# Optimization experiments

Hardware: AMD Instinct MI355X
Metric: run time of the kernel (lower is better)

Reference implementation:

```python
import jax, jax.numpy as jnp
import numpy as np

ALPHA = 0.2  # LeakyReLU negative slope
B, L, FIN, FOUT = 128, 512, 128, 128

def setup_inputs() -> dict:
    key = jax.random.key(0)
    k1, k2, k3, k4, k5 = jax.random.split(key, 5)
    h = jax.random.normal(k1, (B, L, FIN), jnp.float32)
    W = jax.random.normal(k2, (FIN, FOUT), jnp.float32) * (1.0 / np.sqrt(FIN))
    a = jax.random.normal(k3, (2 * FOUT,), jnp.float32) * (1.0 / np.sqrt(2 * FOUT))
    edge_bias = jax.random.normal(k4, (B, L, L), jnp.float32) * 0.1
    adj_mask = jax.random.uniform(k5, (L, L)) > 0.3
    adj_mask = adj_mask | jnp.eye(L, dtype=bool)  # self-loops avoid fully-masked rows
    return {"h": h, "W": W, "a": a, "edge_bias": edge_bias, "adj_mask": adj_mask}

def reference(h, W, a, edge_bias, adj_mask):
    # Wh: [B, L, Fout]
    Wh = jnp.einsum('blf,fo->blo', h, W)
    Fout = W.shape[1]
    # a([Wh_i, Wh_j]) == Wh_i @ a[:Fout] + Wh_j @ a[Fout:]  (avoids O(B*L*L*2F) concat)
    ei = Wh @ a[:Fout]   # [B, L]  (target i contribution)
    ej = Wh @ a[Fout:]   # [B, L]  (source j contribution)
    e = jax.nn.leaky_relu(ei[:, :, None] + ej[:, None, :], ALPHA) + edge_bias  # [B, L, L]
    e = jnp.where(adj_mask[None, :, :], e, -jnp.inf)
    att = jax.nn.softmax(e, axis=-1)  # dropout=0.0 -> identity
    h_prime = jnp.einsum('bij,bjo->bio', att, Wh)  # [B, L, Fout]
    return jax.nn.elu(h_prime)  # concat=True branch
```

## Files before the change

### kernel.cpp

```cpp
#include <hip/hip_runtime.h>
#include <string.h>

#define ALPHA 0.2f

typedef short short8 __attribute__((ext_vector_type(8)));
typedef float floatx4 __attribute__((ext_vector_type(4)));
typedef unsigned short ushort8 __attribute__((ext_vector_type(8)));

__device__ inline unsigned short f2bf(float f) {
    unsigned int v; __builtin_memcpy(&v, &f, 4);
    v = v + 0x7FFFu + ((v >> 16) & 1u);
    return (unsigned short)(v >> 16);
}
__device__ inline float bf2f(unsigned short u) {
    unsigned int v = ((unsigned int)u) << 16;
    float f; __builtin_memcpy(&f, &v, 4); return f;
}

__global__ __launch_bounds__(256) void wh_kernel(const float* __restrict__ h,
                                                 const float* __restrict__ W,
                                                 const float* __restrict__ a,
                                                 unsigned short* __restrict__ wht,
                                                 float* __restrict__ ei,
                                                 float* __restrict__ ej)
{
    __shared__ __align__(16) unsigned short w_t[128][136];
    __shared__ __align__(16) unsigned short out_s[128][136];
    const int tid  = threadIdx.x;
    const int lane = tid & 63;
    const int wv   = tid >> 6;
    const int quad = lane >> 4;
    const int l16  = lane & 15;
    const int r0   = blockIdx.x * 128;
    const int b    = r0 >> 9;
    const int jb   = r0 & 511;

    for (int k = 0; k < 64; ++k) {
        int idx = k * 256 + tid;
        w_t[idx & 127][idx >> 7] = f2bf(W[idx]);
    }
    float a1v[8], a2v[8];
    for (int n = 0; n < 8; ++n) {
        a1v[n] = a[n * 16 + l16];
        a2v[n] = a[128 + n * 16 + l16];
    }
    __syncthreads();

    floatx4 acc[2][8];
    for (int m = 0; m < 2; ++m)
        for (int n = 0; n < 8; ++n) acc[m][n] = (floatx4)0.f;

    for (int kk = 0; kk < 4; ++kk) {
        short8 afr[2];
        for (int m = 0; m < 2; ++m) {
            int r = r0 + wv * 32 + m * 16 + l16;
            const float* src = h + r * 128 + kk * 32 + quad * 8;
            short8 t;
            for (int e = 0; e < 8; ++e) t[e] = (short)f2bf(src[e]);
            afr[m] = t;
        }
        for (int n = 0; n < 8; ++n) {
            short8 bfr = *(const short8*)(&w_t[n * 16 + l16][kk * 32 + quad * 8]);
            for (int m = 0; m < 2; ++m)
                acc[m][n] = __builtin_amdgcn_mfma_f32_16x16x32_bf16(afr[m], bfr, acc[m][n], 0, 0, 0);
        }
    }

    for (int m = 0; m < 2; ++m)
        for (int r = 0; r < 4; ++r) {
            float si = 0.f, sj = 0.f;
            for (int n = 0; n < 8; ++n) {
                float v = acc[m][n][r];
                si += v * a1v[n];
                sj += v * a2v[n];
            }
            for (int off = 8; off; off >>= 1) {
                si += __shfl_xor(si, off);
                sj += __shfl_xor(sj, off);
            }
            if (l16 == 0) {
                int il = wv * 32 + m * 16 + quad * 4 + r;
                ei[b * 512 + jb + il] = si;
                ej[b * 512 + jb + il] = sj;
            }
        }

    for (int m = 0; m < 2; ++m)
        for (int n = 0; n < 8; ++n)
            for (int r = 0; r < 4; ++r)
                out_s[wv * 32 + m * 16 + quad * 4 + r][n * 16 + l16] = f2bf(acc[m][n][r]);
    __syncthreads();

    for (int it = 0; it < 8; ++it) {
        int vid = it * 256 + tid;
        int o   = vid >> 4;
        int jv  = (vid & 15) * 8;
        ushort8 tmp;
        for (int e = 0; e < 8; ++e) tmp[e] = out_s[jv + e][o];
        *(ushort8*)(wht + b * 65536 + o * 512 + jb + jv) = tmp;
    }
}

__global__ __launch_bounds__(256) void attn_kernel(const unsigned short* __restrict__ wht,
                                                   const float* __restrict__ ei,
                                                   const float* __restrict__ ej,
                                                   const float* __restrict__ bias,
                                                   const int* __restrict__ adj,
                                                   float* __restrict__ out)
{
    __shared__ __align__(16) unsigned short p_s[32][520];
    __shared__ __align__(16) unsigned short wh_s[128][136];
    __shared__ float ej_s[512];
    __shared__ float ei_s[32];
    __shared__ float s_row[32];

    const int tid  = threadIdx.x;
    const int lane = tid & 63;
    const int wv   = tid >> 6;
    const int quad = lane >> 4;
    const int l16  = lane & 15;
    const int b    = blockIdx.x >> 4;
    const int i0   = (blockIdx.x & 15) * 32;

    ej_s[tid]       = ej[b * 512 + tid];
    ej_s[256 + tid] = ej[b * 512 + 256 + tid];
    if (tid < 32) ei_s[tid] = ei[b * 512 + i0 + tid];
    __syncthreads();

    for (int rr = 0; rr < 8; ++rr) {
        int il = wv * 8 + rr;
        int ig = i0 + il;
        float eiv = ei_s[il];
        const float* brow = bias + (size_t)(((b << 9) + ig)) * 512;
        const int* arow = adj + (ig << 9);
        float e8[8];
        float mx = -1e30f;
        for (int q = 0; q < 8; ++q) {
            int j = q * 64 + lane;
            float x = eiv + ej_s[j];
            x = x > 0.f ? x : ALPHA * x;
            x += brow[j];
            if (arow[j] == 0) x = -1e30f;
            e8[q] = x;
            mx = fmaxf(mx, x);
        }
        for (int off = 32; off; off >>= 1) mx = fmaxf(mx, __shfl_xor(mx, off));
        float sm = 0.f;
        for (int q = 0; q < 8; ++q) {
            float p = __expf(e8[q] - mx);
            p_s[il][q * 64 + lane] = f2bf(p);
            sm += p;
        }
        for (int off = 32; off; off >>= 1) sm += __shfl_xor(sm, off);
        if (lane == 0) s_row[il] = sm;
    }
    __syncthreads();

    floatx4 acc[2][2];
    for (int m = 0; m < 2; ++m)
        for (int n = 0; n < 2; ++n) acc[m][n] = (floatx4)0.f;

    for (int kc = 0; kc < 4; ++kc) {
        __syncthreads();
        for (int it = 0; it < 8; ++it) {
            int vid = it * 256 + tid;
            int o   = vid >> 4;
            int jv  = (vid & 15) * 8;
            *(ushort8*)&wh_s[o][jv] =
                *(const ushort8*)(wht + b * 65536 + o * 512 + kc * 128 + jv);
        }
        __syncthreads();
        for (int ks = 0; ks < 4; ++ks) {
            int ko = ks * 32 + quad * 8;
            short8 af[2], bfv[2];
            for (int m = 0; m < 2; ++m)
                af[m] = *(const short8*)&p_s[m * 16 + l16][kc * 128 + ko];
            for (int n = 0; n < 2; ++n)
                bfv[n] = *(const short8*)&wh_s[wv * 32 + n * 16 + l16][ko];
            for (int m = 0; m < 2; ++m)
                for (int n = 0; n < 2; ++n)
                    acc[m][n] = __builtin_amdgcn_mfma_f32_16x16x32_bf16(af[m], bfv[n], acc[m][n], 0, 0, 0);
        }
    }

    for (int m = 0; m < 2; ++m)
        for (int n = 0; n < 2; ++n)
            for (int r = 0; r < 4; ++r) {
                int il = m * 16 + quad * 4 + r;
                int o  = wv * 32 + n * 16 + l16;
                float v = acc[m][n][r] / s_row[il];
                v = v > 0.f ? v : (__expf(v) - 1.f);
                out[(((b << 9) + i0 + il) << 7) + o] = v;
            }
}

extern "C" void kernel_launch(void* const* d_in, const int* in_sizes, int n_in,
                              void* d_out, int out_size, void* d_ws, size_t ws_size,
                              hipStream_t stream)
{
    const float* h    = (const float*)d_in[0];
    const float* W    = (const float*)d_in[1];
    const float* a    = (const float*)d_in[2];
    const float* bias = (const float*)d_in[3];
    const int*   adj  = (const int*)d_in[4];
    float*       out  = (float*)d_out;

    unsigned short* wht = (unsigned short*)d_ws;
    float* ei = (float*)((char*)d_ws + 16777216);
    float* ej = ei + 65536;

    hipLaunchKernelGGL(wh_kernel,   dim3(512),  dim3(256), 0, stream, h, W, a, wht, ei, ej);
    hipLaunchKernelGGL(attn_kernel, dim3(2048), dim3(256), 0, stream, wht, ei, ej, bias, adj, out);
}
```

Before: 269.5 us.

## Vectorize and prefetch bias/mask loads, read Wh directly from global in attention

In the attention kernel, each lane now holds four contiguous columns per row. The edge-bias and adjacency rows are read as 16-byte vectors and prefetched one row ahead, and ej is kept in registers instead of shared memory. The P·Wh MFMA loop now reads Wh fragments straight from global memory (expected to hit L2) rather than staging tiles in LDS, which removes the per-chunk barriers. The projection kernel is reoriented to compute Wh^T tiles, so results are written without an LDS transpose. The trade-offs are scalar 2-byte global stores of Wh and more global-load latency exposed inside the MFMA loop.

```diff
diff --git a/kernel.cpp b/kernel.cpp
--- a/kernel.cpp
+++ b/kernel.cpp
@@ -5,16 +5,13 @@
 
 typedef short short8 __attribute__((ext_vector_type(8)));
 typedef float floatx4 __attribute__((ext_vector_type(4)));
-typedef unsigned short ushort8 __attribute__((ext_vector_type(8)));
+typedef int intx4 __attribute__((ext_vector_type(4)));
+typedef unsigned short ushort4v __attribute__((ext_vector_type(4)));
 
 __device__ inline unsigned short f2bf(float f) {
     unsigned int v; __builtin_memcpy(&v, &f, 4);
     v = v + 0x7FFFu + ((v >> 16) & 1u);
     return (unsigned short)(v >> 16);
-}
-__device__ inline float bf2f(unsigned short u) {
-    unsigned int v = ((unsigned int)u) << 16;
-    float f; __builtin_memcpy(&f, &v, 4); return f;
 }
 
 __global__ __launch_bounds__(256) void wh_kernel(const float* __restrict__ h,
@@ -24,8 +21,9 @@
                                                  float* __restrict__ ei,
                                                  float* __restrict__ ej)
 {
-    __shared__ __align__(16) unsigned short w_t[128][136];
-    __shared__ __align__(16) unsigned short out_s[128][136];
+    __shared__ __align__(16) unsigned short h_s[128][136];
+    __shared__ __align__(16) unsigned short w_s[128][136];
+    __shared__ float a_s[256];
     const int tid  = threadIdx.x;
     const int lane = tid & 63;
     const int wv   = tid >> 6;
@@ -35,82 +33,73 @@
     const int b    = r0 >> 9;
     const int jb   = r0 & 511;
 
-    for (int k = 0; k < 64; ++k) {
-        int idx = k * 256 + tid;
-        w_t[idx & 127][idx >> 7] = f2bf(W[idx]);
-    }
-    float a1v[8], a2v[8];
-    for (int n = 0; n < 8; ++n) {
-        a1v[n] = a[n * 16 + l16];
-        a2v[n] = a[128 + n * 16 + l16];
-    }
+    const float* hbase = h + (size_t)r0 * 128;
+    for (int it = 0; it < 16; ++it) {
+        int idx4 = it * 256 + tid;
+        floatx4 v = *(const floatx4*)(hbase + idx4 * 4);
+        int row = idx4 >> 5;
+        int col = (idx4 & 31) * 4;
+        ushort4v u;
+        for (int e = 0; e < 4; ++e) u[e] = f2bf(v[e]);
+        *(ushort4v*)&h_s[row][col] = u;
+    }
+    for (int it = 0; it < 64; ++it) {
+        int idx = it * 256 + tid;
+        w_s[idx & 127][idx >> 7] = f2bf(W[idx]);
+    }
+    a_s[tid] = a[tid];
     __syncthreads();
 
-    floatx4 acc[2][8];
-    for (int m = 0; m < 2; ++m)
-        for (int n = 0; n < 8; ++n) acc[m][n] = (floatx4)0.f;
+    floatx4 acc[8][2];
+    for (int mo = 0; mo < 8; ++mo)
+        for (int n = 0; n < 2; ++n) acc[mo][n] = (floatx4)0.f;
 
     for (int kk = 0; kk < 4; ++kk) {
-        short8 afr[2];
-        for (int m = 0; m < 2; ++m) {
-            int r = r0 + wv * 32 + m * 16 + l16;
-            const float* src = h + r * 128 + kk * 32 + quad * 8;
-            short8 t;
-            for (int e = 0; e < 8; ++e) t[e] = (short)f2bf(src[e]);
-            afr[m] = t;
-        }
-        for (int n = 0; n < 8; ++n) {
-            short8 bfr = *(const short8*)(&w_t[n * 16 + l16][kk * 32 + quad * 8]);
-            for (int m = 0; m < 2; ++m)
-                acc[m][n] = __builtin_amdgcn_mfma_f32_16x16x32_bf16(afr[m], bfr, acc[m][n], 0, 0, 0);
-        }
-    }
-
-    for (int m = 0; m < 2; ++m)
-        for (int r = 0; r < 4; ++r) {
-            float si = 0.f, sj = 0.f;
-            for (int n = 0; n < 8; ++n) {
-                float v = acc[m][n][r];
-                si += v * a1v[n];
-                sj += v * a2v[n];
+        short8 bfr[2];
+        for (int n = 0; n < 2; ++n)
+            bfr[n] = *(const short8*)&h_s[wv * 32 + n * 16 + l16][kk * 32 + quad * 8];
+        for (int mo = 0; mo < 8; ++mo) {
+            short8 afr = *(const short8*)&w_s[mo * 16 + l16][kk * 32 + quad * 8];
+            acc[mo][0] = __builtin_amdgcn_mfma_f32_16x16x32_bf16(afr, bfr[0], acc[mo][0], 0, 0, 0);
+            acc[mo][1] = __builtin_amdgcn_mfma_f32_16x16x32_bf16(afr, bfr[1], acc[mo][1], 0, 0, 0);
+        }
+    }
+
+    for (int n = 0; n < 2; ++n) {
+        float si = 0.f, sj = 0.f;
+        for (int mo = 0; mo < 8; ++mo)
+            for (int r = 0; r < 4; ++r) {
+                int o = mo * 16 + quad * 4 + r;
+                float v = acc[mo][n][r];
+                si += v * a_s[o];
+                sj += v * a_s[128 + o];
             }
-            for (int off = 8; off; off >>= 1) {
-                si += __shfl_xor(si, off);
-                sj += __shfl_xor(sj, off);
+        si += __shfl_xor(si, 16); si += __shfl_xor(si, 32);
+        sj += __shfl_xor(sj, 16); sj += __shfl_xor(sj, 32);
+        if (quad == 0) {
+            int j = jb + wv * 32 + n * 16 + l16;
+            ei[b * 512 + j] = si;
+            ej[b * 512 + j] = sj;
+        }
+    }
+
+    for (int mo = 0; mo < 8; ++mo)
+        for (int n = 0; n < 2; ++n)
+            for (int r = 0; r < 4; ++r) {
+                int o = mo * 16 + quad * 4 + r;
+                int j = jb + wv * 32 + n * 16 + l16;
+                wht[(size_t)b * 65536 + o * 512 + j] = f2bf(acc[mo][n][r]);
             }
-            if (l16 == 0) {
-                int il = wv * 32 + m * 16 + quad * 4 + r;
-                ei[b * 512 + jb + il] = si;
-                ej[b * 512 + jb + il] = sj;
-            }
-        }
-
-    for (int m = 0; m < 2; ++m)
-        for (int n = 0; n < 8; ++n)
-            for (int r = 0; r < 4; ++r)
-                out_s[wv * 32 + m * 16 + quad * 4 + r][n * 16 + l16] = f2bf(acc[m][n][r]);
-    __syncthreads();
-
-    for (int it = 0; it < 8; ++it) {
-        int vid = it * 256 + tid;
-        int o   = vid >> 4;
-        int jv  = (vid & 15) * 8;
-        ushort8 tmp;
-        for (int e = 0; e < 8; ++e) tmp[e] = out_s[jv + e][o];
-        *(ushort8*)(wht + b * 65536 + o * 512 + jb + jv) = tmp;
-    }
-}
-
-__global__ __launch_bounds__(256) void attn_kernel(const unsigned short* __restrict__ wht,
-                                                   const float* __restrict__ ei,
-                                                   const float* __restrict__ ej,
-                                                   const float* __restrict__ bias,
-                                                   const int* __restrict__ adj,
-                                                   float* __restrict__ out)
+}
+
+__global__ __launch_bounds__(256, 4) void attn_kernel(const unsigned short* __restrict__ wht,
+                                                      const float* __restrict__ ei,
+                                                      const float* __restrict__ ej,
+                                                      const float* __restrict__ bias,
+                                                      const int* __restrict__ adj,
+                                                      float* __restrict__ out)
 {
     __shared__ __align__(16) unsigned short p_s[32][520];
-    __shared__ __align__(16) unsigned short wh_s[128][136];
-    __shared__ float ej_s[512];
     __shared__ float ei_s[32];
     __shared__ float s_row[32];
 
@@ -122,37 +111,56 @@
     const int b    = blockIdx.x >> 4;
     const int i0   = (blockIdx.x & 15) * 32;
 
-    ej_s[tid]       = ej[b * 512 + tid];
-    ej_s[256 + tid] = ej[b * 512 + 256 + tid];
+    const floatx4 ejv0 = *(const floatx4*)(ej + b * 512 + lane * 4);
+    const floatx4 ejv1 = *(const floatx4*)(ej + b * 512 + 256 + lane * 4);
     if (tid < 32) ei_s[tid] = ei[b * 512 + i0 + tid];
     __syncthreads();
 
+    const float* bp = bias + ((size_t)(b * 512 + i0 + wv * 8)) * 512;
+    const int*   ap = adj + (i0 + wv * 8) * 512;
+    floatx4 bb0 = *(const floatx4*)(bp + lane * 4);
+    floatx4 bb1 = *(const floatx4*)(bp + 256 + lane * 4);
+    intx4   mm0 = *(const intx4*)(ap + lane * 4);
+    intx4   mm1 = *(const intx4*)(ap + 256 + lane * 4);
+
     for (int rr = 0; rr < 8; ++rr) {
-        int il = wv * 8 + rr;
-        int ig = i0 + il;
-        float eiv = ei_s[il];
-        const float* brow = bias + (size_t)(((b << 9) + ig)) * 512;
-        const int* arow = adj + (ig << 9);
-        float e8[8];
-        float mx = -1e30f;
-        for (int q = 0; q < 8; ++q) {
-            int j = q * 64 + lane;
-            float x = eiv + ej_s[j];
+        floatx4 nb0, nb1; intx4 nm0, nm1;
+        if (rr < 7) {
+            nb0 = *(const floatx4*)(bp + 512 + lane * 4);
+            nb1 = *(const floatx4*)(bp + 768 + lane * 4);
+            nm0 = *(const intx4*)(ap + 512 + lane * 4);
+            nm1 = *(const intx4*)(ap + 768 + lane * 4);
+        }
+        const int il = wv * 8 + rr;
+        const float eiv = ei_s[il];
+        float xs[8];
+        for (int e = 0; e < 4; ++e) {
+            float x = eiv + ejv0[e];
             x = x > 0.f ? x : ALPHA * x;
-            x += brow[j];
-            if (arow[j] == 0) x = -1e30f;
-            e8[q] = x;
-            mx = fmaxf(mx, x);
-        }
+            x += bb0[e];
+            if (mm0[e] == 0) x = -1e30f;
+            xs[e] = x;
+        }
+        for (int e = 0; e < 4; ++e) {
+            float x = eiv + ejv1[e];
+            x = x > 0.f ? x : ALPHA * x;
+            x += bb1[e];
+            if (mm1[e] == 0) x = -1e30f;
+            xs[4 + e] = x;
+        }
+        float mx = xs[0];
+        for (int e = 1; e < 8; ++e) mx = fmaxf(mx, xs[e]);
         for (int off = 32; off; off >>= 1) mx = fmaxf(mx, __shfl_xor(mx, off));
         float sm = 0.f;
-        for (int q = 0; q < 8; ++q) {
-            float p = __expf(e8[q] - mx);
-            p_s[il][q * 64 + lane] = f2bf(p);
-            sm += p;
-        }
+        ushort4v p0, p1;
+        for (int e = 0; e < 4; ++e) { float p = __expf(xs[e] - mx);     sm += p; p0[e] = f2bf(p); }
+        for (int e = 0; e < 4; ++e) { float p = __expf(xs[4 + e] - mx); sm += p; p1[e] = f2bf(p); }
+        *(ushort4v*)&p_s[il][lane * 4]       = p0;
+        *(ushort4v*)&p_s[il][256 + lane * 4] = p1;
         for (int off = 32; off; off >>= 1) sm += __shfl_xor(sm, off);
         if (lane == 0) s_row[il] = sm;
+        bb0 = nb0; bb1 = nb1; mm0 = nm0; mm1 = nm1;
+        bp += 512; ap += 512;
     }
     __syncthreads();
 
@@ -160,27 +168,18 @@
     for (int m = 0; m < 2; ++m)
         for (int n = 0; n < 2; ++n) acc[m][n] = (floatx4)0.f;
 
-    for (int kc = 0; kc < 4; ++kc) {
-        __syncthreads();
-        for (int it = 0; it < 8; ++it) {
-            int vid = it * 256 + tid;
-            int o   = vid >> 4;
-            int jv  = (vid & 15) * 8;
-            *(ushort8*)&wh_s[o][jv] =
-                *(const ushort8*)(wht + b * 65536 + o * 512 + kc * 128 + jv);
-        }
-        __syncthreads();
-        for (int ks = 0; ks < 4; ++ks) {
-            int ko = ks * 32 + quad * 8;
-            short8 af[2], bfv[2];
-            for (int m = 0; m < 2; ++m)
-                af[m] = *(const short8*)&p_s[m * 16 + l16][kc * 128 + ko];
-            for (int n = 0; n < 2; ++n)
-                bfv[n] = *(const short8*)&wh_s[wv * 32 + n * 16 + l16][ko];
-            for (int m = 0; m < 2; ++m)
-                for (int n = 0; n < 2; ++n)
-                    acc[m][n] = __builtin_amdgcn_mfma_f32_16x16x32_bf16(af[m], bfv[n], acc[m][n], 0, 0, 0);
-        }
+    const unsigned short* wbase = wht + (size_t)b * 65536;
+#pragma unroll 4
+    for (int k16 = 0; k16 < 16; ++k16) {
+        int ko = k16 * 32 + quad * 8;
+        short8 af0 = *(const short8*)&p_s[l16][ko];
+        short8 af1 = *(const short8*)&p_s[16 + l16][ko];
+        short8 bf0 = *(const short8*)(wbase + (wv * 32 + l16) * 512 + ko);
+        short8 bf1 = *(const short8*)(wbase + (wv * 32 + 16 + l16) * 512 + ko);
+        acc[0][0] = __builtin_amdgcn_mfma_f32_16x16x32_bf16(af0, bf0, acc[0][0], 0, 0, 0);
+        acc[0][1] = __builtin_amdgcn_mfma_f32_16x16x32_bf16(af0, bf1, acc[0][1], 0, 0, 0);
+        acc[1][0] = __builtin_amdgcn_mfma_f32_16x16x32_bf16(af1, bf0, acc[1][0], 0, 0, 0);
+        acc[1][1] = __builtin_amdgcn_mfma_f32_16x16x32_bf16(af1, bf1, acc[1][1], 0, 0, 0);
     }
 
     for (int m = 0; m < 2; ++m)
@@ -190,7 +189,7 @@
                 int o  = wv * 32 + n * 16 + l16;
                 float v = acc[m][n][r] / s_row[il];
                 v = v > 0.f ? v : (__expf(v) - 1.f);
-                out[(((b << 9) + i0 + il) << 7) + o] = v;
+                out[((size_t)(b * 512 + i0 + il)) * 128 + o] = v;
             }
 }
 
```

After: 264.1 us. 2.0% less time.
